# Optimization experiments

Hardware: AMD Instinct MI355X
Metric: run time of the kernel (lower is better)

The kernel has to match this reference:

```python
import jax, jax.numpy as jnp
import numpy as np

N = 512
D = 128        # d_model
DE = 128       # d_edge
DFF = 2048
H = 8          # n_head
DH = D // H
LN_EPS = 1e-5


def layer_norm(x, g, b):
    m = jnp.mean(x, axis=-1, keepdims=True)
    v = jnp.mean((x - m) ** 2, axis=-1, keepdims=True)
    return (x - m) * jax.lax.rsqrt(v + LN_EPS) * g + b


def setup_inputs() -> dict:
    key = jax.random.key(0)
    ks = jax.random.split(key, 20)
    s = 0.02
    d = {
        "node": jax.random.normal(ks[0], (N, D), jnp.float32),
        "edge": jax.random.normal(ks[1], (N, N, DE), jnp.float32),
        "edge_mask": jnp.zeros((N, N), dtype=bool),
        # proj_memory: Linear(d_edge+2*d_model -> d_model) split by concat blocks [edge|src|tar]
        "w_mem_e": s * jax.random.normal(ks[2], (DE, D), jnp.float32),
        "w_mem_s": s * jax.random.normal(ks[3], (D, D), jnp.float32),
        "w_mem_t": s * jax.random.normal(ks[4], (D, D), jnp.float32),
        "b_mem": jnp.zeros((D,), jnp.float32),
        "g_ln_mem": jnp.ones((D,), jnp.float32),
        "b_ln_mem": jnp.zeros((D,), jnp.float32),
        # proj_edge: Linear(d_model -> d_edge) + LN, then norm_edge
        "w_pe": s * jax.random.normal(ks[5], (D, DE), jnp.float32),
        "b_pe": jnp.zeros((DE,), jnp.float32),
        "g_ln_pe": jnp.ones((DE,), jnp.float32),
        "b_ln_pe": jnp.zeros((DE,), jnp.float32),
        "g_ln_edge": jnp.ones((DE,), jnp.float32),
        "b_ln_edge": jnp.zeros((DE,), jnp.float32),
        # MHA in/out projections
        "wq": s * jax.random.normal(ks[6], (D, D), jnp.float32),
        "bq": jnp.zeros((D,), jnp.float32),
        "wk": s * jax.random.normal(ks[7], (D, D), jnp.float32),
        "bk": jnp.zeros((D,), jnp.float32),
        "wv": s * jax.random.normal(ks[8], (D, D), jnp.float32),
        "bv": jnp.zeros((D,), jnp.float32),
        "wo": s * jax.random.normal(ks[9], (D, D), jnp.float32),
        "bo": jnp.zeros((D,), jnp.float32),
        "g_ln2": jnp.ones((D,), jnp.float32),
        "b_ln2": jnp.zeros((D,), jnp.float32),
        # FFN
        "w_ff1": s * jax.random.normal(ks[10], (D, DFF), jnp.float32),
        "b_ff1": jnp.zeros((DFF,), jnp.float32),
        "w_ff2": s * jax.random.normal(ks[11], (DFF, D), jnp.float32),
        "b_ff2": jnp.zeros((D,), jnp.float32),
        "g_ln3": jnp.ones((D,), jnp.float32),
        "b_ln3": jnp.zeros((D,), jnp.float32),
    }
    return d


def reference(node, edge, edge_mask,
              w_mem_e, w_mem_s, w_mem_t, b_mem, g_ln_mem, b_ln_mem,
              w_pe, b_pe, g_ln_pe, b_ln_pe, g_ln_edge, b_ln_edge,
              wq, bq, wk, bk, wv, bv, wo, bo, g_ln2, b_ln2,
              w_ff1, b_ff1, w_ff2, b_ff2, g_ln3, b_ln3):
    # ---- _build_memory ----
    # torch concat order [edge, src_x, tar_x]: src_x[i,j]=node[j], tar_x[i,j]=node[i].
    # Avoid materializing the (N,N,2D+DE) concat: split the linear by block.
    mem_pre = (jnp.einsum('ijd,df->ijf', edge, w_mem_e)
               + (node @ w_mem_s)[None, :, :]
               + (node @ w_mem_t)[:, None, :]
               + b_mem)                                   # (N, N, D)
    memory = jax.nn.relu(layer_norm(mem_pre, g_ln_mem, b_ln_mem))
    edge_upd = jax.nn.relu(layer_norm(memory @ w_pe + b_pe, g_ln_pe, b_ln_pe))
    edge_new = layer_norm(edge + edge_upd, g_ln_edge, b_ln_edge)  # (N, N, DE)

    # ---- MHA: query len 1, batch N, key/value = memory (src_len=N, batch=N) ----
    q = (node @ wq + bq).reshape(N, H, DH)                # (Nb, H, DH)
    k = (jnp.einsum('snd,df->snf', memory, wk) + bk).reshape(N, N, H, DH)  # (S, Nb, H, DH)
    v = (jnp.einsum('snd,df->snf', memory, wv) + bv).reshape(N, N, H, DH)
    scores = jnp.einsum('nhd,snhd->nhs', q, k) / jnp.sqrt(jnp.float32(DH))  # (Nb, H, S)
    scores = jnp.where(edge_mask[:, None, :], jnp.finfo(scores.dtype).min, scores)
    attn = jax.nn.softmax(scores, axis=-1)
    ctx = jnp.einsum('nhs,snhd->nhd', attn, v).reshape(N, D)
    x_prime = ctx @ wo + bo                               # (N, D)

    # ---- residual + norms + FFN ----
    x = layer_norm(node + x_prime, g_ln2, b_ln2)
    ff = jax.nn.relu(x @ w_ff1 + b_ff1) @ w_ff2 + b_ff2
    x = layer_norm(x + ff, g_ln3, b_ln3)
    return (x, edge_new)
```

## Files before the change

### kernel.cpp

```cpp
#include <hip/hip_runtime.h>

#define NN 512
#define DD 128
#define DFF 2048
#define HH 8
#define DHH 16

typedef __attribute__((ext_vector_type(8))) short short8;
typedef __attribute__((ext_vector_type(4))) float f32x4;

static __device__ __forceinline__ float bf2f(ushort u) {
    union { unsigned int i; float f; } v; v.i = ((unsigned int)u) << 16; return v.f;
}
static __device__ __forceinline__ ushort f2bf(float f) {
    union { float f; unsigned int i; } v; v.f = f;
    unsigned int x = v.i;
    return (ushort)((x + 0x7fffu + ((x >> 16) & 1u)) >> 16);
}

static __device__ __forceinline__ int probe_f32(const void* p) {
    return (((const ushort*)p)[0] == 0) ? 1 : 0;
}
static __device__ __forceinline__ float ld(const void* p, size_t i, int f32) {
    return f32 ? ((const float*)p)[i] : bf2f(((const ushort*)p)[i]);
}
static __device__ __forceinline__ void st(void* p, size_t i, float v, int f32) {
    if (f32) ((float*)p)[i] = v; else ((ushort*)p)[i] = f2bf(v);
}

static __device__ __forceinline__ ushort* mem_row_ptr(void* out_base, void* wsmem,
                                                      int big, int f32, int r) {
    if (big) return (ushort*)wsmem + (size_t)r * DD;
    char* b = (char*)out_base;
    return f32 ? (ushort*)(b + (size_t)4*NN*DD + (size_t)r*4*DD)
               : (ushort*)(b + (size_t)2*NN*DD + (size_t)r*2*DD);
}

static __device__ __forceinline__ int swz(int row, int b) {
    return row*256 + (b ^ ((row & 15) << 4));
}

static __device__ __forceinline__ float2 ln_tree(float v, float* red, float* red2) {
    const int t = threadIdx.x;
    __syncthreads();
    red[t] = v; red2[t] = v * v;
    __syncthreads();
    for (int s = 64; s > 0; s >>= 1) {
        if (t < s) { red[t] += red[t + s]; red2[t] += red2[t + s]; }
        __syncthreads();
    }
    float mean = red[0] * (1.f / 128.f);
    float var  = red2[0] * (1.f / 128.f) - mean * mean;
    float2 r; r.x = mean; r.y = rsqrtf(fmaxf(var, 0.f) + 1e-5f);
    return r;
}

__global__ __launch_bounds__(256) void k_wconv(
    const void* __restrict__ w_mem_e, const void* __restrict__ w_pe,
    const void* __restrict__ dt_probe, ushort* __restrict__ wf)
{
    const int f32 = probe_f32(dt_probe);
    int idx = blockIdx.x * 256 + threadIdx.x;
    const void* W = (idx < 32768) ? w_mem_e : w_pe;
    int rem = idx & 32767;
    int b = rem & 7, lane = (rem >> 3) & 63, ks = (rem >> 9) & 3, tn = rem >> 11;
    int k = ks*32 + (lane >> 4)*8 + b;
    int n = tn*16 + (lane & 15);
    wf[idx] = f2bf(ld(W, (size_t)k*DD + n, f32));
}

__global__ __launch_bounds__(256) void k_wconv2(
    const void* __restrict__ w_ff1, const void* __restrict__ w_ff2,
    const void* __restrict__ dt_probe, ushort* __restrict__ wf)
{
    const int f32 = probe_f32(dt_probe);
    int idx = blockIdx.x * 256 + threadIdx.x;
    if (idx < 262144) {
        int b = idx & 7, lane = (idx >> 3) & 63, ks = (idx >> 9) & 3, ct = idx >> 11;
        int k = ks*32 + (lane >> 4)*8 + b;
        int n = ct*16 + (lane & 15);
        wf[idx] = f2bf(ld(w_ff1, (size_t)k*DFF + n, f32));
    } else {
        int rem = idx - 262144;
        int b = rem & 7, lane = (rem >> 3) & 63, kc = (rem >> 9) & 63, tn = rem >> 15;
        int k = kc*32 + (lane >> 4)*8 + b;
        int n = tn*16 + (lane & 15);
        wf[idx] = f2bf(ld(w_ff2, (size_t)k*DD + n, f32));
    }
}

__global__ __launch_bounds__(128) void k_pre(
    const void* __restrict__ node, const void* __restrict__ w_mem_s,
    const void* __restrict__ w_mem_t, const void* __restrict__ wq,
    const void* __restrict__ bq, const void* __restrict__ wk,
    const void* __restrict__ bk, const void* __restrict__ dt_probe,
    float* __restrict__ a_s, float* __restrict__ a_t,
    float* __restrict__ qw, float* __restrict__ qb)
{
    const int f32 = probe_f32(dt_probe);
    const int n = blockIdx.x;
    const int t = threadIdx.x;
    __shared__ float nr[DD];
    __shared__ float qr[DD];
    nr[t] = ld(node, (size_t)n*DD + t, f32);
    __syncthreads();
    float s_acc = 0.f, t_acc = 0.f, q_acc = ld(bq, t, f32);
    for (int k = 0; k < DD; ++k) {
        float nv = nr[k];
        s_acc += nv * ld(w_mem_s, (size_t)k*DD + t, f32);
        t_acc += nv * ld(w_mem_t, (size_t)k*DD + t, f32);
        q_acc += nv * ld(wq,      (size_t)k*DD + t, f32);
    }
    a_s[(size_t)n*DD + t] = s_acc;
    a_t[(size_t)n*DD + t] = t_acc;
    qr[t] = q_acc;
    __syncthreads();
    for (int h = 0; h < HH; ++h) {
        float acc = 0.f;
        #pragma unroll
        for (int dh = 0; dh < DHH; ++dh)
            acc += qr[h*DHH + dh] * ld(wk, (size_t)t*DD + h*DHH + dh, f32);
        qw[((size_t)n*HH + h)*DD + t] = acc;
    }
    if (t < HH) {
        float acc = 0.f;
        #pragma unroll
        for (int dh = 0; dh < DHH; ++dh)
            acc += qr[t*DHH + dh] * ld(bk, (size_t)t*DHH + dh, f32);
        qb[(size_t)n*HH + t] = acc;
    }
}

__global__ __launch_bounds__(256) void k_mem_mfma(
    const void* __restrict__ edge, const ushort* __restrict__ wfe,
    const void* __restrict__ b_mem, const void* __restrict__ g1,
    const void* __restrict__ b1, const void* __restrict__ dt_probe,
    const float* __restrict__ a_s, const float* __restrict__ a_t,
    void* __restrict__ out_base, void* __restrict__ wsmem, int big)
{
    const int f32 = probe_f32(dt_probe);
    const int t = threadIdx.x;
    const int r0 = blockIdx.x * 64;
    const int i0 = r0 >> 9;
    const int j0 = r0 & (NN - 1);

    __shared__ __align__(16) ushort tile[64*128];

    {
        const int row = t >> 2;
        const int c0  = (t & 3) * 32;
        if (f32) {
            const float4* gp = (const float4*)((const float*)edge
                               + (size_t)(r0 + row)*DD + c0);
            #pragma unroll
            for (int q = 0; q < 4; ++q) {
                float4 v0 = gp[2*q], v1 = gp[2*q+1];
                short8 u;
                u[0]=(short)f2bf(v0.x); u[1]=(short)f2bf(v0.y);
                u[2]=(short)f2bf(v0.z); u[3]=(short)f2bf(v0.w);
                u[4]=(short)f2bf(v1.x); u[5]=(short)f2bf(v1.y);
                u[6]=(short)f2bf(v1.z); u[7]=(short)f2bf(v1.w);
                *(short8*)((char*)tile + swz(row, c0*2 + q*16)) = u;
            }
        } else {
            const short8* gp = (const short8*)((const ushort*)edge
                               + (size_t)(r0 + row)*DD + c0);
            #pragma unroll
            for (int q = 0; q < 4; ++q)
                *(short8*)((char*)tile + swz(row, c0*2 + q*16)) = gp[q];
        }
    }
    __syncthreads();

    const int lane = t & 63, w = t >> 6;
    const int rowbase = w * 16;
    const int l15 = lane & 15, g = lane >> 4;

    short8 afr[4];
    #pragma unroll
    for (int ks = 0; ks < 4; ++ks)
        afr[ks] = *(const short8*)((const char*)tile
                   + swz(rowbase + l15, ks*64 + g*16));

    f32x4 acc[8];
    #pragma unroll
    for (int tn = 0; tn < 8; ++tn) {
        acc[tn][0]=0.f; acc[tn][1]=0.f; acc[tn][2]=0.f; acc[tn][3]=0.f;
    }

    #pragma unroll
    for (int tn = 0; tn < 8; ++tn) {
        #pragma unroll
        for (int ks = 0; ks < 4; ++ks) {
            short8 bfr = *(const short8*)(wfe + ((tn*4 + ks)*64 + lane)*8);
            acc[tn] = __builtin_amdgcn_mfma_f32_16x16x32_bf16(afr[ks], bfr,
                                                              acc[tn], 0, 0, 0);
        }
    }

    float atb[8], gg[8], bb[8];
    #pragma unroll
    for (int tn = 0; tn < 8; ++tn) {
        int c = tn*16 + l15;
        atb[tn] = a_t[(size_t)i0*DD + c] + ld(b_mem, c, f32);
        gg[tn]  = ld(g1, c, f32);
        bb[tn]  = ld(b1, c, f32);
    }

    float sum[4], sq[4];
    #pragma unroll
    for (int reg = 0; reg < 4; ++reg) {
        const int rr = rowbase + 4*g + reg;
        float s = 0.f, qq = 0.f;
        #pragma unroll
        for (int tn = 0; tn < 8; ++tn) {
            float v = acc[tn][reg]
                    + a_s[(size_t)(j0 + rr)*DD + tn*16 + l15] + atb[tn];
            acc[tn][reg] = v;
            s += v; qq += v*v;
        }
        sum[reg] = s; sq[reg] = qq;
    }
    #pragma unroll
    for (int m = 1; m < 16; m <<= 1) {
        #pragma unroll
        for (int reg = 0; reg < 4; ++reg) {
            sum[reg] += __shfl_xor(sum[reg], m, 64);
            sq[reg]  += __shfl_xor(sq[reg],  m, 64);
        }
    }

    #pragma unroll
    for (int reg = 0; reg < 4; ++reg) {
        const int rr = rowbase + 4*g + reg;
        float mean = sum[reg] * (1.f/128.f);
        float var  = sq[reg] * (1.f/128.f) - mean*mean;
        float rstd = rsqrtf(fmaxf(var, 0.f) + 1e-5f);
        #pragma unroll
        for (int tn = 0; tn < 8; ++tn) {
            float v = fmaxf((acc[tn][reg]-mean)*rstd*gg[tn] + bb[tn], 0.f);
            *(ushort*)((char*)tile + swz(rr, (tn*16 + l15)*2)) = f2bf(v);
        }
    }
    __syncthreads();

    {
        const int crow = rowbase + l15;
        ushort* dst = mem_row_ptr(out_base, wsmem, big, f32, r0 + crow);
        #pragma unroll
        for (int q = 0; q < 4; ++q) {
            short8 u = *(const short8*)((const char*)tile
                        + swz(crow, g*64 + q*16));
            *(short8*)(dst + g*32 + q*8) = u;
        }
    }
}

__global__ __launch_bounds__(256) void k_attn(
    const float* __restrict__ qw, const float* __restrict__ qb,
    const unsigned char* __restrict__ mask,
    const void* __restrict__ wv_w, const void* __restrict__ bv,
    const void* __restrict__ dt_probe,
    void* __restrict__ out_base, void* __restrict__ wsmem, int big,
    float* __restrict__ ctx)
{
    const int f32 = probe_f32(dt_probe);
    const int n = blockIdx.x;
    const int t = threadIdx.x;

    __shared__ __align__(16) float qwl[HH*DD];
    __shared__ float qbl[HH];
    __shared__ __align__(16) float sc[HH*NN];
    __shared__ __align__(16) float msub[64*132];
    __shared__ float srd[HH*33];
    __shared__ __align__(16) float pml[HH*DD];

    #pragma unroll
    for (int u = 0; u < 4; ++u) qwl[t + 256*u] = qw[(size_t)n*HH*DD + t + 256*u];
    if (t < HH) qbl[t] = qb[(size_t)n*HH + t];
    __syncthreads();

    const int h0 = t >> 6;
    const int sl = t & 63;

    for (int s0 = 0; s0 < NN; s0 += 64) {
        __syncthreads();
        #pragma unroll
        for (int u = 0; u < 4; ++u) {
            int c = u*256 + t;
            int row = c >> 4, sub = c & 15;
            const ushort* src = mem_row_ptr(out_base, wsmem, big, f32,
                                            (s0 + row)*NN + n) + sub*8;
            short8 uv = *(const short8*)src;
            float4 x0, x1;
            x0.x=bf2f((ushort)uv[0]); x0.y=bf2f((ushort)uv[1]);
            x0.z=bf2f((ushort)uv[2]); x0.w=bf2f((ushort)uv[3]);
            x1.x=bf2f((ushort)uv[4]); x1.y=bf2f((ushort)uv[5]);
            x1.z=bf2f((ushort)uv[6]); x1.w=bf2f((ushort)uv[7]);
            float* d = msub + row*132 + sub*8;
            *(float4*)d = x0; *(float4*)(d + 4) = x1;
        }
        __syncthreads();
        float a0 = 0.f, a1 = 0.f;
        const float* mrow = msub + sl*132;
        const float* q0p = qwl + h0*DD;
        const float* q1p = qwl + (h0+4)*DD;
        for (int d = 0; d < DD; d += 4) {
            float4 mv = *(const float4*)(mrow + d);
            float4 qa = *(const float4*)(q0p + d);
            float4 qc = *(const float4*)(q1p + d);
            a0 += mv.x*qa.x + mv.y*qa.y + mv.z*qa.z + mv.w*qa.w;
            a1 += mv.x*qc.x + mv.y*qc.y + mv.z*qc.z + mv.w*qc.w;
        }
        int s = s0 + sl;
        int mk = mask[(size_t)n*NN + s] != 0;
        sc[h0*NN + s]     = mk ? -1.0e30f : 0.25f*(a0 + qbl[h0]);
        sc[(h0+4)*NN + s] = mk ? -1.0e30f : 0.25f*(a1 + qbl[h0+4]);
    }
    __syncthreads();

    {
        const int h = t >> 5, l = t & 31;
        float mx = -1.0e30f;
        for (int k = 0; k < 16; ++k) mx = fmaxf(mx, sc[h*NN + l + 32*k]);
        srd[h*33 + l] = mx;
        __syncthreads();
        for (int s = 16; s > 0; s >>= 1) {
            if (l < s) srd[h*33 + l] = fmaxf(srd[h*33 + l], srd[h*33 + l + s]);
            __syncthreads();
        }
        mx = srd[h*33];
        __syncthreads();
        float sum = 0.f;
        for (int k = 0; k < 16; ++k) {
            float e = __expf(sc[h*NN + l + 32*k] - mx);
            sc[h*NN + l + 32*k] = e;
            sum += e;
        }
        srd[h*33 + l] = sum;
        __syncthreads();
        for (int s = 16; s > 0; s >>= 1) {
            if (l < s) srd[h*33 + l] += srd[h*33 + l + s];
            __syncthreads();
        }
        float inv = 1.f / srd[h*33];
        for (int k = 0; k < 16; ++k) sc[h*NN + l + 32*k] *= inv;
    }
    __syncthreads();

    const int h2 = t >> 5, d4 = (t & 31) * 4;
    float4 acc2; acc2.x = 0.f; acc2.y = 0.f; acc2.z = 0.f; acc2.w = 0.f;
    for (int s0 = 0; s0 < NN; s0 += 64) {
        __syncthreads();
        #pragma unroll
        for (int u = 0; u < 4; ++u) {
            int c = u*256 + t;
            int row = c >> 4, sub = c & 15;
            const ushort* src = mem_row_ptr(out_base, wsmem, big, f32,
                                            (s0 + row)*NN + n) + sub*8;
            short8 uv = *(const short8*)src;
            float4 x0, x1;
            x0.x=bf2f((ushort)uv[0]); x0.y=bf2f((ushort)uv[1]);
            x0.z=bf2f((ushort)uv[2]); x0.w=bf2f((ushort)uv[3]);
            x1.x=bf2f((ushort)uv[4]); x1.y=bf2f((ushort)uv[5]);
            x1.z=bf2f((ushort)uv[6]); x1.w=bf2f((ushort)uv[7]);
            float* d = msub + row*132 + sub*8;
            *(float4*)d = x0; *(float4*)(d + 4) = x1;
        }
        __syncthreads();
        for (int s = 0; s < 64; ++s) {
            float wgt = sc[h2*NN + s0 + s];
            float4 mv = *(const float4*)(msub + s*132 + d4);
            acc2.x += wgt*mv.x; acc2.y += wgt*mv.y;
            acc2.z += wgt*mv.z; acc2.w += wgt*mv.w;
        }
    }
    *(float4*)(pml + h2*DD + d4) = acc2;
    __syncthreads();

    if (t < DD) {
        int h = t >> 4;
        float c = ld(bv, t, f32);
        const float* pr = pml + h*DD;
        for (int d = 0; d < DD; ++d)
            c += pr[d] * ld(wv_w, (size_t)d*DD + t, f32);
        ctx[(size_t)n*DD + t] = c;
    }
}

__global__ __launch_bounds__(256) void k_edge_mfma(
    const void* __restrict__ edge, const ushort* __restrict__ wfp,
    const void* __restrict__ b_pe, const void* __restrict__ g2,
    const void* __restrict__ b2, const void* __restrict__ g3,
    const void* __restrict__ b3, const void* __restrict__ dt_probe,
    void* __restrict__ out_base, void* __restrict__ wsmem, int big)
{
    const int f32 = probe_f32(dt_probe);
    const int t = threadIdx.x;
    const int r0 = blockIdx.x * 64;

    __shared__ __align__(16) ushort tile[64*128];
    __shared__ __align__(16) float  etile[64*132];

    {
        const int row = t >> 2, ch = t & 3;
        const ushort* src = mem_row_ptr(out_base, wsmem, big, f32, r0 + row);
        #pragma unroll
        for (int q = 0; q < 4; ++q) {
            short8 u = *(const short8*)(src + ch*32 + q*8);
            *(short8*)((char*)tile + swz(row, ch*64 + q*16)) = u;
        }
        float* ed = etile + row*132 + ch*32;
        if (f32) {
            const float4* gp = (const float4*)((const float*)edge
                               + (size_t)(r0 + row)*DD + ch*32);
            #pragma unroll
            for (int q = 0; q < 8; ++q) ((float4*)ed)[q] = gp[q];
        } else {
            const ushort* gp = (const ushort*)edge + (size_t)(r0 + row)*DD + ch*32;
            #pragma unroll
            for (int q = 0; q < 4; ++q) {
                short8 u = *(const short8*)(gp + q*8);
                float4 x0, x1;
                x0.x=bf2f((ushort)u[0]); x0.y=bf2f((ushort)u[1]);
                x0.z=bf2f((ushort)u[2]); x0.w=bf2f((ushort)u[3]);
                x1.x=bf2f((ushort)u[4]); x1.y=bf2f((ushort)u[5]);
                x1.z=bf2f((ushort)u[6]); x1.w=bf2f((ushort)u[7]);
                ((float4*)ed)[2*q] = x0; ((float4*)ed)[2*q+1] = x1;
            }
        }
    }
    __syncthreads();

    const int lane = t & 63, w = t >> 6;
    const int rowbase = w * 16;
    const int l15 = lane & 15, g = lane >> 4;

    short8 afr[4];
    #pragma unroll
    for (int ks = 0; ks < 4; ++ks)
        afr[ks] = *(const short8*)((const char*)tile
                   + swz(rowbase + l15, ks*64 + g*16));

    f32x4 acc[8];
    #pragma unroll
    for (int tn = 0; tn < 8; ++tn) {
        acc[tn][0]=0.f; acc[tn][1]=0.f; acc[tn][2]=0.f; acc[tn][3]=0.f;
    }
    #pragma unroll
    for (int tn = 0; tn < 8; ++tn) {
        #pragma unroll
        for (int ks = 0; ks < 4; ++ks) {
            short8 bfr = *(const short8*)(wfp + ((tn*4 + ks)*64 + lane)*8);
            acc[tn] = __builtin_amdgcn_mfma_f32_16x16x32_bf16(afr[ks], bfr,
                                                              acc[tn], 0, 0, 0);
        }
    }

    float bpe[8], gg2[8], bb2[8], gg3[8], bb3[8];
    #pragma unroll
    for (int tn = 0; tn < 8; ++tn) {
        int c = tn*16 + l15;
        bpe[tn] = ld(b_pe, c, f32);
        gg2[tn] = ld(g2, c, f32); bb2[tn] = ld(b2, c, f32);
        gg3[tn] = ld(g3, c, f32); bb3[tn] = ld(b3, c, f32);
    }

    float sum[4], sq[4];
    #pragma unroll
    for (int reg = 0; reg < 4; ++reg) {
        float s = 0.f, qq = 0.f;
        #pragma unroll
        for (int tn = 0; tn < 8; ++tn) {
            float v = acc[tn][reg] + bpe[tn];
            acc[tn][reg] = v;
            s += v; qq += v*v;
        }
        sum[reg] = s; sq[reg] = qq;
    }
    #pragma unroll
    for (int m = 1; m < 16; m <<= 1) {
        #pragma unroll
        for (int reg = 0; reg < 4; ++reg) {
            sum[reg] += __shfl_xor(sum[reg], m, 64);
            sq[reg]  += __shfl_xor(sq[reg],  m, 64);
        }
    }

    float sum2[4], sq2[4];
    #pragma unroll
    for (int reg = 0; reg < 4; ++reg) {
        const int rr = rowbase + 4*g + reg;
        float mean = sum[reg] * (1.f/128.f);
        float var  = sq[reg] * (1.f/128.f) - mean*mean;
        float rstd = rsqrtf(fmaxf(var, 0.f) + 1e-5f);
        float s2 = 0.f, q2 = 0.f;
        #pragma unroll
        for (int tn = 0; tn < 8; ++tn) {
            float upd = fmaxf((acc[tn][reg]-mean)*rstd*gg2[tn] + bb2[tn], 0.f);
            float y = etile[rr*132 + tn*16 + l15] + upd;
            acc[tn][reg] = y;
            s2 += y; q2 += y*y;
        }
        sum2[reg] = s2; sq2[reg] = q2;
    }
    #pragma unroll
    for (int m = 1; m < 16; m <<= 1) {
        #pragma unroll
        for (int reg = 0; reg < 4; ++reg) {
            sum2[reg] += __shfl_xor(sum2[reg], m, 64);
            sq2[reg]  += __shfl_xor(sq2[reg],  m, 64);
        }
    }
    #pragma unroll
    for (int reg = 0; reg < 4; ++reg) {
        const int rr = rowbase + 4*g + reg;
        float mean = sum2[reg] * (1.f/128.f);
        float var  = sq2[reg] * (1.f/128.f) - mean*mean;
        float rstd = rsqrtf(fmaxf(var, 0.f) + 1e-5f);
        #pragma unroll
        for (int tn = 0; tn < 8; ++tn)
            etile[rr*132 + tn*16 + l15] =
                (acc[tn][reg]-mean)*rstd*gg3[tn] + bb3[tn];
    }
    __syncthreads();

    {
        const int crow = rowbase + l15;
        const size_t rbase = (size_t)NN*DD + (size_t)(r0 + crow)*DD + g*32;
        const float* srcl = etile + crow*132 + g*32;
        if (f32) {
            float* dst = (float*)out_base + rbase;
            #pragma unroll
            for (int q = 0; q < 8; ++q)
                *(float4*)(dst + q*4) = *(const float4*)(srcl + q*4);
        } else {
            ushort* dst = (ushort*)out_base + rbase;
            #pragma unroll
            for (int q = 0; q < 4; ++q) {
                float4 v0 = *(const float4*)(srcl + q*8);
                float4 v1 = *(const float4*)(srcl + q*8 + 4);
                short8 u;
                u[0]=(short)f2bf(v0.x); u[1]=(short)f2bf(v0.y);
                u[2]=(short)f2bf(v0.z); u[3]=(short)f2bf(v0.w);
                u[4]=(short)f2bf(v1.x); u[5]=(short)f2bf(v1.y);
                u[6]=(short)f2bf(v1.z); u[7]=(short)f2bf(v1.w);
                *(short8*)(dst + q*8) = u;
            }
        }
    }
}

__global__ __launch_bounds__(128) void k_post1(
    const float* __restrict__ ctx, const void* __restrict__ wo,
    const void* __restrict__ bo, const void* __restrict__ node,
    const void* __restrict__ g2, const void* __restrict__ b2,
    const void* __restrict__ dt_probe, float* __restrict__ xbuf,
    float* __restrict__ out_acc)
{
    const int f32 = probe_f32(dt_probe);
    const int n = blockIdx.x;
    const int t = threadIdx.x;
    __shared__ float cr[DD];
    __shared__ float red[DD], red2[DD];

    out_acc[(size_t)n*DD + t] = 0.f;

    cr[t] = ctx[(size_t)n*DD + t];
    __syncthreads();
    float xp = ld(bo, t, f32);
    for (int k = 0; k < DD; ++k)
        xp += cr[k] * ld(wo, (size_t)k*DD + t, f32);
    float x0 = ld(node, (size_t)n*DD + t, f32) + xp;
    float2 st1 = ln_tree(x0, red, red2);
    xbuf[(size_t)n*DD + t] = (x0 - st1.x) * st1.y * ld(g2, t, f32) + ld(b2, t, f32);
}

__global__ __launch_bounds__(256) void k_ffn_sk(
    const float* __restrict__ xbuf, const ushort* __restrict__ wf1,
    const ushort* __restrict__ wf2, const void* __restrict__ b1,
    const void* __restrict__ dt_probe, float* __restrict__ out_acc)
{
    const int f32 = probe_f32(dt_probe);
    const int t = threadIdx.x;
    const int rt = blockIdx.x & 7;
    const int kt = blockIdx.x >> 3;
    const int r0 = rt * 64;

    __shared__ __align__(16) ushort xt[64*128];
    __shared__ __align__(16) ushort ht[64*128];

    {
        const int row = t >> 2, c0 = (t & 3) * 32;
        const float4* gp = (const float4*)(xbuf + (size_t)(r0 + row)*DD + c0);
        #pragma unroll
        for (int q = 0; q < 4; ++q) {
            float4 v0 = gp[2*q], v1 = gp[2*q+1];
            short8 u;
            u[0]=(short)f2bf(v0.x); u[1]=(short)f2bf(v0.y);
            u[2]=(short)f2bf(v0.z); u[3]=(short)f2bf(v0.w);
            u[4]=(short)f2bf(v1.x); u[5]=(short)f2bf(v1.y);
            u[6]=(short)f2bf(v1.z); u[7]=(short)f2bf(v1.w);
            *(short8*)((char*)xt + swz(row, c0*2 + q*16)) = u;
        }
    }
    __syncthreads();

    const int lane = t & 63, w = t >> 6;
    const int rowbase = w * 16;
    const int l15 = lane & 15, g = lane >> 4;

    short8 afr[4];
    #pragma unroll
    for (int ks = 0; ks < 4; ++ks)
        afr[ks] = *(const short8*)((const char*)xt
                   + swz(rowbase + l15, ks*64 + g*16));

    f32x4 hacc[8];
    #pragma unroll
    for (int tn = 0; tn < 8; ++tn) {
        hacc[tn][0]=0.f; hacc[tn][1]=0.f; hacc[tn][2]=0.f; hacc[tn][3]=0.f;
    }
    #pragma unroll
    for (int tn = 0; tn < 8; ++tn) {
        #pragma unroll
        for (int ks = 0; ks < 4; ++ks) {
            short8 bfr = *(const short8*)(wf1
                          + (((size_t)(kt*8 + tn)*4 + ks)*64 + lane)*8);
            hacc[tn] = __builtin_amdgcn_mfma_f32_16x16x32_bf16(afr[ks], bfr,
                                                               hacc[tn], 0, 0, 0);
        }
    }
    float b1v[8];
    #pragma unroll
    for (int tn = 0; tn < 8; ++tn)
        b1v[tn] = ld(b1, kt*128 + tn*16 + l15, f32);
    #pragma unroll
    for (int reg = 0; reg < 4; ++reg) {
        const int rr = rowbase + 4*g + reg;
        #pragma unroll
        for (int tn = 0; tn < 8; ++tn) {
            float v = fmaxf(hacc[tn][reg] + b1v[tn], 0.f);
            *(ushort*)((char*)ht + swz(rr, (tn*16 + l15)*2)) = f2bf(v);
        }
    }
    __syncthreads();

    short8 afr2[4];
    #pragma unroll
    for (int ks = 0; ks < 4; ++ks)
        afr2[ks] = *(const short8*)((const char*)ht
                    + swz(rowbase + l15, ks*64 + g*16));
    f32x4 oacc[8];
    #pragma unroll
    for (int tn = 0; tn < 8; ++tn) {
        oacc[tn][0]=0.f; oacc[tn][1]=0.f; oacc[tn][2]=0.f; oacc[tn][3]=0.f;
    }
    #pragma unroll
    for (int tn = 0; tn < 8; ++tn) {
        #pragma unroll
        for (int ks = 0; ks < 4; ++ks) {
            short8 bfr = *(const short8*)(wf2
                          + (((size_t)tn*64 + kt*4 + ks)*64 + lane)*8);
            oacc[tn] = __builtin_amdgcn_mfma_f32_16x16x32_bf16(afr2[ks], bfr,
                                                               oacc[tn], 0, 0, 0);
        }
    }

    #pragma unroll
    for (int reg = 0; reg < 4; ++reg) {
        const int rr = rowbase + 4*g + reg;
        #pragma unroll
        for (int tn = 0; tn < 8; ++tn)
            unsafeAtomicAdd(&out_acc[(size_t)(r0 + rr)*DD + tn*16 + l15],
                            oacc[tn][reg]);
    }
}

__global__ __launch_bounds__(128) void k_ffn_fin(
    const float* __restrict__ xbuf, const float* __restrict__ out_acc,
    const void* __restrict__ b2f, const void* __restrict__ g3,
    const void* __restrict__ b3, const void* __restrict__ dt_probe,
    void* __restrict__ out_base)
{
    const int f32 = probe_f32(dt_probe);
    const int n = blockIdx.x;
    const int t = threadIdx.x;
    __shared__ float red[DD], red2[DD];

    float y = xbuf[(size_t)n*DD + t] + out_acc[(size_t)n*DD + t]
            + ld(b2f, t, f32);
    float2 st2 = ln_tree(y, red, red2);
    float outv = (y - st2.x) * st2.y * ld(g3, t, f32) + ld(b3, t, f32);
    st(out_base, (size_t)n*DD + t, outv, f32);
}

extern "C" void kernel_launch(void* const* d_in, const int* in_sizes, int n_in,
                              void* d_out, int out_size, void* d_ws, size_t ws_size,
                              hipStream_t stream)
{
    const void* node     = d_in[0];
    const void* edge     = d_in[1];
    const unsigned char* mask = (const unsigned char*)d_in[2];
    const void* w_mem_e  = d_in[3];
    const void* w_mem_s  = d_in[4];
    const void* w_mem_t  = d_in[5];
    const void* b_mem    = d_in[6];
    const void* g_ln_mem = d_in[7];
    const void* b_ln_mem = d_in[8];
    const void* w_pe     = d_in[9];
    const void* b_pe     = d_in[10];
    const void* g_ln_pe  = d_in[11];
    const void* b_ln_pe  = d_in[12];
    const void* g_ln_edge= d_in[13];
    const void* b_ln_edge= d_in[14];
    const void* wq       = d_in[15];
    const void* bq       = d_in[16];
    const void* wk       = d_in[17];
    const void* bk       = d_in[18];
    const void* wv       = d_in[19];
    const void* bv       = d_in[20];
    const void* wo       = d_in[21];
    const void* bo       = d_in[22];
    const void* g_ln2    = d_in[23];
    const void* b_ln2    = d_in[24];
    const void* w_ff1    = d_in[25];
    const void* b_ff1    = d_in[26];
    const void* w_ff2    = d_in[27];
    const void* b_ff2    = d_in[28];
    const void* g_ln3    = d_in[29];
    const void* b_ln3    = d_in[30];

    float* wsf  = (float*)d_ws;
    float* a_s  = wsf;
    float* a_t  = wsf +  65536;
    float* qw   = wsf + 131072;
    float* qb   = wsf + 655360;
    float* ctxp = wsf + 659456;
    ushort* wf1 = (ushort*)d_ws;
    ushort* wf2 = (ushort*)d_ws + 262144;
    float* xbuf = wsf + 262144;
    float* oaccp= wsf + 327680;
    void*  wsmem = (char*)d_ws + (size_t)4*1024*1024;
    int big = (ws_size >= (size_t)72*1024*1024) ? 1 : 0;

    const void* probe = g_ln_mem;

    ushort* wfe = (ushort*)d_out;
    ushort* wfp = wfe + 32768;

    k_wconv<<<256, 256, 0, stream>>>(w_mem_e, w_pe, probe, wfe);
    k_pre<<<NN, 128, 0, stream>>>(node, w_mem_s, w_mem_t, wq, bq, wk, bk, probe,
                                  a_s, a_t, qw, qb);
    k_mem_mfma<<<(NN*NN)/64, 256, 0, stream>>>(edge, wfe, b_mem, g_ln_mem,
                                               b_ln_mem, probe, a_s, a_t,
                                               d_out, wsmem, big);
    k_attn<<<NN, 256, 0, stream>>>(qw, qb, mask, wv, bv, probe,
                                   d_out, wsmem, big, ctxp);
    k_wconv2<<<2048, 256, 0, stream>>>(w_ff1, w_ff2, probe, wf1);
    k_edge_mfma<<<(NN*NN)/64, 256, 0, stream>>>(edge, wfp, b_pe, g_ln_pe,
                                                b_ln_pe, g_ln_edge, b_ln_edge,
                                                probe, d_out, wsmem, big);
    k_post1<<<NN, 128, 0, stream>>>(ctxp, wo, bo, node, g_ln2, b_ln2,
                                    probe, xbuf, oaccp);
    k_ffn_sk<<<128, 256, 0, stream>>>(xbuf, wf1, wf2, b_ff1, probe, oaccp);
    k_ffn_fin<<<NN, 128, 0, stream>>>(xbuf, oaccp, b_ff2, g_ln3, b_ln3,
                                      probe, d_out);
}
```

Baseline: 625.3 us.

## Fuse memory projection and edge-update kernels into one MFMA pass

Adds k_fused, which computes the memory projection, LayerNorm and ReLU for a 64-row tile and then applies the proj_edge GEMM, both LayerNorms and the residual in the same block. The memory tile stays in LDS instead of being re-read from the workspace by a separate kernel. The edge A-fragments are now loaded straight from global memory rather than staged through LDS, and the edge residual is re-read element-wise from global. The fused path runs only when the workspace is large; otherwise the old two-kernel path is kept. A pack8 helper deduplicates bf16 packing code.

```diff
diff --git a/kernel.cpp b/kernel.cpp
--- a/kernel.cpp
+++ b/kernel.cpp
@@ -16,6 +16,14 @@
     union { float f; unsigned int i; } v; v.f = f;
     unsigned int x = v.i;
     return (ushort)((x + 0x7fffu + ((x >> 16) & 1u)) >> 16);
+}
+static __device__ __forceinline__ short8 pack8(float4 v0, float4 v1) {
+    short8 u;
+    u[0]=(short)f2bf(v0.x); u[1]=(short)f2bf(v0.y);
+    u[2]=(short)f2bf(v0.z); u[3]=(short)f2bf(v0.w);
+    u[4]=(short)f2bf(v1.x); u[5]=(short)f2bf(v1.y);
+    u[6]=(short)f2bf(v1.z); u[7]=(short)f2bf(v1.w);
+    return u;
 }
 
 static __device__ __forceinline__ int probe_f32(const void* p) {
@@ -131,6 +139,205 @@
     }
 }
 
+__global__ __launch_bounds__(256) void k_fused(
+    const void* __restrict__ edge, const ushort* __restrict__ wfe,
+    const ushort* __restrict__ wfp, const void* __restrict__ b_mem,
+    const void* __restrict__ g1, const void* __restrict__ b1,
+    const void* __restrict__ b_pe, const void* __restrict__ g2,
+    const void* __restrict__ b2, const void* __restrict__ g3,
+    const void* __restrict__ b3, const void* __restrict__ dt_probe,
+    const float* __restrict__ a_s, const float* __restrict__ a_t,
+    void* __restrict__ out_base, ushort* __restrict__ memws)
+{
+    const int f32 = probe_f32(dt_probe);
+    const int t = threadIdx.x;
+    const int r0 = blockIdx.x * 64;
+    const int i0 = r0 >> 9;
+    const int j0 = r0 & (NN - 1);
+
+    __shared__ __align__(16) ushort tile[64*128];
+
+    const int lane = t & 63, w = t >> 6;
+    const int rowbase = w * 16;
+    const int l15 = lane & 15, g = lane >> 4;
+    const int arow = r0 + rowbase + l15;
+
+    short8 afr[4];
+    if (f32) {
+        const float* ep = (const float*)edge + (size_t)arow*DD;
+        #pragma unroll
+        for (int ks = 0; ks < 4; ++ks) {
+            float4 v0 = *(const float4*)(ep + ks*32 + g*8);
+            float4 v1 = *(const float4*)(ep + ks*32 + g*8 + 4);
+            afr[ks] = pack8(v0, v1);
+        }
+    } else {
+        const ushort* ep = (const ushort*)edge + (size_t)arow*DD;
+        #pragma unroll
+        for (int ks = 0; ks < 4; ++ks)
+            afr[ks] = *(const short8*)(ep + ks*32 + g*8);
+    }
+
+    f32x4 acc[8];
+    #pragma unroll
+    for (int tn = 0; tn < 8; ++tn) {
+        acc[tn][0]=0.f; acc[tn][1]=0.f; acc[tn][2]=0.f; acc[tn][3]=0.f;
+    }
+    #pragma unroll
+    for (int tn = 0; tn < 8; ++tn) {
+        #pragma unroll
+        for (int ks = 0; ks < 4; ++ks) {
+            short8 bfr = *(const short8*)(wfe + ((tn*4 + ks)*64 + lane)*8);
+            acc[tn] = __builtin_amdgcn_mfma_f32_16x16x32_bf16(afr[ks], bfr,
+                                                              acc[tn], 0, 0, 0);
+        }
+    }
+
+    float atb[8], gg[8], bb[8];
+    #pragma unroll
+    for (int tn = 0; tn < 8; ++tn) {
+        int c = tn*16 + l15;
+        atb[tn] = a_t[(size_t)i0*DD + c] + ld(b_mem, c, f32);
+        gg[tn]  = ld(g1, c, f32);
+        bb[tn]  = ld(b1, c, f32);
+    }
+
+    float sum[4], sq[4];
+    #pragma unroll
+    for (int reg = 0; reg < 4; ++reg) {
+        const int rr = rowbase + 4*g + reg;
+        float s = 0.f, qq = 0.f;
+        #pragma unroll
+        for (int tn = 0; tn < 8; ++tn) {
+            float v = acc[tn][reg]
+                    + a_s[(size_t)(j0 + rr)*DD + tn*16 + l15] + atb[tn];
+            acc[tn][reg] = v;
+            s += v; qq += v*v;
+        }
+        sum[reg] = s; sq[reg] = qq;
+    }
+    #pragma unroll
+    for (int m = 1; m < 16; m <<= 1) {
+        #pragma unroll
+        for (int reg = 0; reg < 4; ++reg) {
+            sum[reg] += __shfl_xor(sum[reg], m, 64);
+            sq[reg]  += __shfl_xor(sq[reg],  m, 64);
+        }
+    }
+    #pragma unroll
+    for (int reg = 0; reg < 4; ++reg) {
+        const int rr = rowbase + 4*g + reg;
+        float mean = sum[reg] * (1.f/128.f);
+        float var  = sq[reg] * (1.f/128.f) - mean*mean;
+        float rstd = rsqrtf(fmaxf(var, 0.f) + 1e-5f);
+        #pragma unroll
+        for (int tn = 0; tn < 8; ++tn) {
+            float v = fmaxf((acc[tn][reg]-mean)*rstd*gg[tn] + bb[tn], 0.f);
+            *(ushort*)((char*)tile + swz(rr, (tn*16 + l15)*2)) = f2bf(v);
+        }
+    }
+
+    {
+        const int crow = rowbase + l15;
+        ushort* dst = memws + (size_t)(r0 + crow)*DD;
+        #pragma unroll
+        for (int q = 0; q < 4; ++q)
+            *(short8*)(dst + g*32 + q*8) =
+                *(const short8*)((const char*)tile + swz(crow, g*64 + q*16));
+    }
+
+    short8 afr2[4];
+    #pragma unroll
+    for (int ks = 0; ks < 4; ++ks)
+        afr2[ks] = *(const short8*)((const char*)tile
+                    + swz(rowbase + l15, ks*64 + g*16));
+
+    f32x4 acc2[8];
+    #pragma unroll
+    for (int tn = 0; tn < 8; ++tn) {
+        acc2[tn][0]=0.f; acc2[tn][1]=0.f; acc2[tn][2]=0.f; acc2[tn][3]=0.f;
+    }
+    #pragma unroll
+    for (int tn = 0; tn < 8; ++tn) {
+        #pragma unroll
+        for (int ks = 0; ks < 4; ++ks) {
+            short8 bfr = *(const short8*)(wfp + ((tn*4 + ks)*64 + lane)*8);
+            acc2[tn] = __builtin_amdgcn_mfma_f32_16x16x32_bf16(afr2[ks], bfr,
+                                                               acc2[tn], 0, 0, 0);
+        }
+    }
+
+    float bpe[8], gg2[8], bb2[8], gg3v[8], bb3v[8];
+    #pragma unroll
+    for (int tn = 0; tn < 8; ++tn) {
+        int c = tn*16 + l15;
+        bpe[tn]  = ld(b_pe, c, f32);
+        gg2[tn]  = ld(g2, c, f32); bb2[tn] = ld(b2, c, f32);
+        gg3v[tn] = ld(g3, c, f32); bb3v[tn] = ld(b3, c, f32);
+    }
+
+    float s1[4], q1[4];
+    #pragma unroll
+    for (int reg = 0; reg < 4; ++reg) {
+        float s = 0.f, qq = 0.f;
+        #pragma unroll
+        for (int tn = 0; tn < 8; ++tn) {
+            float v = acc2[tn][reg] + bpe[tn];
+            acc2[tn][reg] = v;
+            s += v; qq += v*v;
+        }
+        s1[reg] = s; q1[reg] = qq;
+    }
+    #pragma unroll
+    for (int m = 1; m < 16; m <<= 1) {
+        #pragma unroll
+        for (int reg = 0; reg < 4; ++reg) {
+            s1[reg] += __shfl_xor(s1[reg], m, 64);
+            q1[reg] += __shfl_xor(q1[reg], m, 64);
+        }
+    }
+
+    float s2[4], q2[4];
+    #pragma unroll
+    for (int reg = 0; reg < 4; ++reg) {
+        const int rr = rowbase + 4*g + reg;
+        float mean = s1[reg] * (1.f/128.f);
+        float var  = q1[reg] * (1.f/128.f) - mean*mean;
+        float rstd = rsqrtf(fmaxf(var, 0.f) + 1e-5f);
+        float ss = 0.f, qq = 0.f;
+        #pragma unroll
+        for (int tn = 0; tn < 8; ++tn) {
+            float upd = fmaxf((acc2[tn][reg]-mean)*rstd*gg2[tn] + bb2[tn], 0.f);
+            float ev  = ld(edge, (size_t)(r0 + rr)*DD + tn*16 + l15, f32);
+            float y = ev + upd;
+            acc2[tn][reg] = y;
+            ss += y; qq += y*y;
+        }
+        s2[reg] = ss; q2[reg] = qq;
+    }
+    #pragma unroll
+    for (int m = 1; m < 16; m <<= 1) {
+        #pragma unroll
+        for (int reg = 0; reg < 4; ++reg) {
+            s2[reg] += __shfl_xor(s2[reg], m, 64);
+            q2[reg] += __shfl_xor(q2[reg], m, 64);
+        }
+    }
+    #pragma unroll
+    for (int reg = 0; reg < 4; ++reg) {
+        const int rr = rowbase + 4*g + reg;
+        float mean = s2[reg] * (1.f/128.f);
+        float var  = q2[reg] * (1.f/128.f) - mean*mean;
+        float rstd = rsqrtf(fmaxf(var, 0.f) + 1e-5f);
+        #pragma unroll
+        for (int tn = 0; tn < 8; ++tn) {
+            float outv = (acc2[tn][reg]-mean)*rstd*gg3v[tn] + bb3v[tn];
+            st(out_base, (size_t)NN*DD + (size_t)(r0 + rr)*DD + tn*16 + l15,
+               outv, f32);
+        }
+    }
+}
+
 __global__ __launch_bounds__(256) void k_mem_mfma(
     const void* __restrict__ edge, const ushort* __restrict__ wfe,
     const void* __restrict__ b_mem, const void* __restrict__ g1,
@@ -153,15 +360,9 @@
             const float4* gp = (const float4*)((const float*)edge
                                + (size_t)(r0 + row)*DD + c0);
             #pragma unroll
-            for (int q = 0; q < 4; ++q) {
-                float4 v0 = gp[2*q], v1 = gp[2*q+1];
-                short8 u;
-                u[0]=(short)f2bf(v0.x); u[1]=(short)f2bf(v0.y);
-                u[2]=(short)f2bf(v0.z); u[3]=(short)f2bf(v0.w);
-                u[4]=(short)f2bf(v1.x); u[5]=(short)f2bf(v1.y);
-                u[6]=(short)f2bf(v1.z); u[7]=(short)f2bf(v1.w);
-                *(short8*)((char*)tile + swz(row, c0*2 + q*16)) = u;
-            }
+            for (int q = 0; q < 4; ++q)
+                *(short8*)((char*)tile + swz(row, c0*2 + q*16)) =
+                    pack8(gp[2*q], gp[2*q+1]);
         } else {
             const short8* gp = (const short8*)((const ushort*)edge
                                + (size_t)(r0 + row)*DD + c0);
@@ -187,7 +388,6 @@
     for (int tn = 0; tn < 8; ++tn) {
         acc[tn][0]=0.f; acc[tn][1]=0.f; acc[tn][2]=0.f; acc[tn][3]=0.f;
     }
-
     #pragma unroll
     for (int tn = 0; tn < 8; ++tn) {
         #pragma unroll
@@ -229,7 +429,6 @@
             sq[reg]  += __shfl_xor(sq[reg],  m, 64);
         }
     }
-
     #pragma unroll
     for (int reg = 0; reg < 4; ++reg) {
         const int rr = rowbase + 4*g + reg;
@@ -248,11 +447,9 @@
         const int crow = rowbase + l15;
         ushort* dst = mem_row_ptr(out_base, wsmem, big, f32, r0 + crow);
         #pragma unroll
-        for (int q = 0; q < 4; ++q) {
-            short8 u = *(const short8*)((const char*)tile
-                        + swz(crow, g*64 + q*16));
-            *(short8*)(dst + g*32 + q*8) = u;
-        }
+        for (int q = 0; q < 4; ++q)
+            *(short8*)(dst + g*32 + q*8) =
+                *(const short8*)((const char*)tile + swz(crow, g*64 + q*16));
     }
 }
 
@@ -540,12 +737,7 @@
             for (int q = 0; q < 4; ++q) {
                 float4 v0 = *(const float4*)(srcl + q*8);
                 float4 v1 = *(const float4*)(srcl + q*8 + 4);
-                short8 u;
-                u[0]=(short)f2bf(v0.x); u[1]=(short)f2bf(v0.y);
-                u[2]=(short)f2bf(v0.z); u[3]=(short)f2bf(v0.w);
-                u[4]=(short)f2bf(v1.x); u[5]=(short)f2bf(v1.y);
-                u[6]=(short)f2bf(v1.z); u[7]=(short)f2bf(v1.w);
-                *(short8*)(dst + q*8) = u;
+                *(short8*)(dst + q*8) = pack8(v0, v1);
             }
         }
     }
@@ -594,15 +786,9 @@
         const int row = t >> 2, c0 = (t & 3) * 32;
         const float4* gp = (const float4*)(xbuf + (size_t)(r0 + row)*DD + c0);
         #pragma unroll
-        for (int q = 0; q < 4; ++q) {
-            float4 v0 = gp[2*q], v1 = gp[2*q+1];
-            short8 u;
-            u[0]=(short)f2bf(v0.x); u[1]=(short)f2bf(v0.y);
-            u[2]=(short)f2bf(v0.z); u[3]=(short)f2bf(v0.w);
-            u[4]=(short)f2bf(v1.x); u[5]=(short)f2bf(v1.y);
-            u[6]=(short)f2bf(v1.z); u[7]=(short)f2bf(v1.w);
-            *(short8*)((char*)xt + swz(row, c0*2 + q*16)) = u;
-        }
+        for (int q = 0; q < 4; ++q)
+            *(short8*)((char*)xt + swz(row, c0*2 + q*16)) =
+                pack8(gp[2*q], gp[2*q+1]);
     }
     __syncthreads();
 
@@ -752,15 +938,27 @@
     k_wconv<<<256, 256, 0, stream>>>(w_mem_e, w_pe, probe, wfe);
     k_pre<<<NN, 128, 0, stream>>>(node, w_mem_s, w_mem_t, wq, bq, wk, bk, probe,
                                   a_s, a_t, qw, qb);
-    k_mem_mfma<<<(NN*NN)/64, 256, 0, stream>>>(edge, wfe, b_mem, g_ln_mem,
-                                               b_ln_mem, probe, a_s, a_t,
-                                               d_out, wsmem, big);
-    k_attn<<<NN, 256, 0, stream>>>(qw, qb, mask, wv, bv, probe,
-                                   d_out, wsmem, big, ctxp);
-    k_wconv2<<<2048, 256, 0, stream>>>(w_ff1, w_ff2, probe, wf1);
-    k_edge_mfma<<<(NN*NN)/64, 256, 0, stream>>>(edge, wfp, b_pe, g_ln_pe,
-                                                b_ln_pe, g_ln_edge, b_ln_edge,
-                                                probe, d_out, wsmem, big);
+    if (big) {
+        k_fused<<<(NN*NN)/64, 256, 0, stream>>>(edge, wfe, wfp, b_mem,
+                                                g_ln_mem, b_ln_mem, b_pe,
+                                                g_ln_pe, b_ln_pe, g_ln_edge,
+                                                b_ln_edge, probe, a_s, a_t,
+                                                d_out, (ushort*)wsmem);
+        k_attn<<<NN, 256, 0, stream>>>(qw, qb, mask, wv, bv, probe,
+                                       d_out, wsmem, 1, ctxp);
+        k_wconv2<<<2048, 256, 0, stream>>>(w_ff1, w_ff2, probe, wf1);
+    } else {
+        k_mem_mfma<<<(NN*NN)/64, 256, 0, stream>>>(edge, wfe, b_mem, g_ln_mem,
+                                                   b_ln_mem, probe, a_s, a_t,
+                                                   d_out, wsmem, big);
+        k_attn<<<NN, 256, 0, stream>>>(qw, qb, mask, wv, bv, probe,
+                                       d_out, wsmem, big, ctxp);
+        k_wconv2<<<2048, 256, 0, stream>>>(w_ff1, w_ff2, probe, wf1);
+        k_edge_mfma<<<(NN*NN)/64, 256, 0, stream>>>(edge, wfp, b_pe, g_ln_pe,
+                                                    b_ln_pe, g_ln_edge,
+                                                    b_ln_edge, probe, d_out,
+                                                    wsmem, big);
+    }
     k_post1<<<NN, 128, 0, stream>>>(ctxp, wo, bo, node, g_ln2, b_ln2,
                                     probe, xbuf, oaccp);
     k_ffn_sk<<<128, 256, 0, stream>>>(xbuf, wf1, wf2, b_ff1, probe, oaccp);
```

Result: faster. 552.1 us (-11.7%).
